# Performance work log

Hardware: AMD Instinct MI355X
Metric: run time of the kernel (lower is better)

## Reference

```python
import jax, jax.numpy as jnp
import numpy as np
import math

D_MODEL = 1024
N_HEADS = 16
D_KV = 64
NUM_BUCKETS = 32
MAX_DISTANCE = 128
BATCH = 4
SEQ = 2048


def _relative_position_bucket(relative_position, num_buckets=NUM_BUCKETS, max_distance=MAX_DISTANCE):
    # bidirectional=True (encoder)
    num_buckets //= 2
    relative_buckets = (relative_position > 0).astype(jnp.int32) * num_buckets
    rp = jnp.abs(relative_position)
    max_exact = num_buckets // 2
    is_small = rp < max_exact
    rp_safe = jnp.maximum(rp, 1)  # avoid log(0); masked by is_small anyway
    rp_if_large = max_exact + (
        jnp.log(rp_safe.astype(jnp.float32) / max_exact)
        / math.log(max_distance / max_exact)
        * (num_buckets - max_exact)
    ).astype(jnp.int32)
    rp_if_large = jnp.minimum(rp_if_large, num_buckets - 1)
    relative_buckets += jnp.where(is_small, rp, rp_if_large)
    return relative_buckets


def compute_bias(rel_bias, q_len, k_len):
    context = jnp.arange(q_len)[:, None]
    memory = jnp.arange(k_len)[None, :]
    buckets = _relative_position_bucket(memory - context)  # [q, k]
    values = rel_bias[buckets]                              # [q, k, h]
    return jnp.transpose(values, (2, 0, 1))[None]           # [1, h, q, k]


def setup_inputs() -> dict:
    key = jax.random.key(0)
    ks = jax.random.split(key, 6)
    s = 1.0 / math.sqrt(D_MODEL)
    return {
        "hidden_states": jax.random.normal(ks[0], (BATCH, SEQ, D_MODEL), jnp.float32),
        "wq": jax.random.normal(ks[1], (D_MODEL, N_HEADS * D_KV), jnp.float32) * s,
        "wk": jax.random.normal(ks[2], (D_MODEL, N_HEADS * D_KV), jnp.float32) * s,
        "wv": jax.random.normal(ks[3], (D_MODEL, N_HEADS * D_KV), jnp.float32) * s,
        "wo": jax.random.normal(ks[4], (N_HEADS * D_KV, D_MODEL), jnp.float32) * s,
        "rel_bias": jax.random.normal(ks[5], (NUM_BUCKETS, N_HEADS), jnp.float32) * 0.5,
    }


def reference(hidden_states, wq, wk, wv, wo, rel_bias):
    B, S, _ = hidden_states.shape

    def shape(x):  # [B,S,H*Dk] -> [B,H,S,Dk]
        return x.reshape(B, S, N_HEADS, D_KV).transpose(0, 2, 1, 3)

    q = shape(hidden_states @ wq)
    k = shape(hidden_states @ wk)
    v = shape(hidden_states @ wv)

    # NOTE: T5 does NOT scale by 1/sqrt(d_kv)
    scores = jnp.einsum("bhqd,bhkd->bhqk", q, k)
    position_bias = compute_bias(rel_bias, S, S)  # [1,H,S,S]
    scores = scores + position_bias
    attn = jax.nn.softmax(scores.astype(jnp.float32), axis=-1).astype(scores.dtype)
    ctx = jnp.einsum("bhqk,bhkd->bhqd", attn, v)
    ctx = ctx.transpose(0, 2, 1, 3).reshape(B, S, N_HEADS * D_KV)
    return ctx @ wo
```

## Files before the change

kernel.cpp:

```cpp
#include <hip/hip_runtime.h>
#include <hip/hip_bf16.h>

typedef unsigned short u16;
typedef unsigned int   u32;
typedef __bf16 bf16x8 __attribute__((ext_vector_type(8)));
typedef float  f32x4  __attribute__((ext_vector_type(4)));
typedef u16    u16x8  __attribute__((ext_vector_type(8)));
typedef u16    u16x4  __attribute__((ext_vector_type(4)));

#define MFMA16(a,b,c) __builtin_amdgcn_mfma_f32_16x16x32_bf16(a,b,c,0,0,0)
#define LOG2E 1.4426950408889634f

__device__ __forceinline__ u16 f2b(float f) {
    u32 u = __builtin_bit_cast(u32, f);
    u32 r = (u + 0x7FFFu + ((u >> 16) & 1u)) >> 16;
    return (u16)r;
}

typedef const __attribute__((address_space(1))) u32* gaddr_t;
typedef __attribute__((address_space(3))) u32*       laddr_t;
__device__ __forceinline__ void gl_lds16(const void* g, void* l) {
    __builtin_amdgcn_global_load_lds((gaddr_t)g, (laddr_t)l, 16, 0, 0);
}

__global__ __launch_bounds__(256) void cast_h_kernel(const float* __restrict__ src,
                                                     u16* __restrict__ dst) {
    int i = (blockIdx.x * 256 + threadIdx.x) * 8;
    float4 a = *(const float4*)(src + i);
    float4 b = *(const float4*)(src + i + 4);
    u16x8 o = { f2b(a.x), f2b(a.y), f2b(a.z), f2b(a.w),
                f2b(b.x), f2b(b.y), f2b(b.z), f2b(b.w) };
    *(u16x8*)(dst + i) = o;
}

__global__ __launch_bounds__(256) void transpose_w_kernel(
        const float* __restrict__ wq, const float* __restrict__ wk,
        const float* __restrict__ wv, const float* __restrict__ wo,
        u16* __restrict__ Wt, u16* __restrict__ Wot) {
    __shared__ u16 tile[64 * 72];
    int g = blockIdx.z;
    const float* src = (g == 0) ? wq : (g == 1) ? wk : (g == 2) ? wv : wo;
    u16* dst = (g < 3) ? (Wt + g * 1048576) : Wot;
    int k0 = blockIdx.x * 64, n0 = blockIdx.y * 64;
    int t = threadIdx.x;
#pragma unroll
    for (int rr = 0; rr < 4; ++rr) {
        int idx = rr * 256 + t;
        int kr = idx >> 4, c = idx & 15;
        float4 v = *(const float4*)(src + (k0 + kr) * 1024 + n0 + c * 4);
        u16x4 o = { f2b(v.x), f2b(v.y), f2b(v.z), f2b(v.w) };
        *(u16x4*)&tile[kr * 72 + c * 4] = o;
    }
    __syncthreads();
#pragma unroll
    for (int rr = 0; rr < 2; ++rr) {
        int idx = rr * 256 + t;
        int n = idx >> 3, c = idx & 7;
        u16x8 o;
#pragma unroll
        for (int j = 0; j < 8; ++j) o[j] = tile[(c * 8 + j) * 72 + n];
        *(u16x8*)(dst + (n0 + n) * 1024 + k0 + c * 8) = o;
    }
}

__global__ __launch_bounds__(256) void bias_kernel(const float* __restrict__ rel_bias,
                                                   float* __restrict__ tab) {
    int i = blockIdx.x * 256 + threadIdx.x;
    int h = i >> 12;
    int idx = i & 4095;
    int delta = idx - 2048;
    int bucket = (delta > 0) ? 16 : 0;
    int rp = delta < 0 ? -delta : delta;
    if (rp < 8) {
        bucket += rp;
    } else {
        double v = log((double)rp / 8.0) / log(16.0) * 8.0;
        int tt = (int)v;
        int b2 = 8 + tt;
        bucket += (b2 < 15) ? b2 : 15;
    }
    tab[h * 4096 + idx] = rel_bias[bucket * 16 + h] * LOG2E;
}

template <int MODE>
__global__ __launch_bounds__(256) void gemm_bt(
        const u16* __restrict__ A, const u16* __restrict__ Bt, int K, int N,
        u16* __restrict__ q_out, u16* __restrict__ k_out, u16* __restrict__ v_out,
        float* __restrict__ f_out) {
    __shared__ u16 As[128 * 32];
    __shared__ u16 Bs[128 * 32];
    int t = threadIdx.x;
    int lane = t & 63, w = t >> 6;
    int wm = w & 1, wn = w >> 1;
    int ln = lane & 15, quad = lane >> 4;
    int m0 = blockIdx.x * 128, n0 = blockIdx.y * 128;
    const u16* Ab = A + m0 * K;
    const u16* Bb = Bt + n0 * K;
    f32x4 acc[4][4] = {};
    int nk = K >> 5;
    for (int kt = 0; kt < nk; ++kt) {
        int k0 = kt * 32;
#pragma unroll
        for (int rr = 0; rr < 2; ++rr) {
            int idx = rr * 256 + t;
            int row = idx >> 2, c = (idx & 3) ^ (row & 3);
            gl_lds16(Ab + row * K + k0 + c * 8, ((char*)As) + idx * 16);
            gl_lds16(Bb + row * K + k0 + c * 8, ((char*)Bs) + idx * 16);
        }
        __syncthreads();
        bf16x8 af[4], bfr[4];
#pragma unroll
        for (int mb = 0; mb < 4; ++mb) {
            int row = wm * 64 + mb * 16 + ln;
            af[mb] = *(const bf16x8*)&As[row * 32 + ((quad ^ (row & 3)) << 3)];
        }
#pragma unroll
        for (int nb = 0; nb < 4; ++nb) {
            int row = wn * 64 + nb * 16 + ln;
            bfr[nb] = *(const bf16x8*)&Bs[row * 32 + ((quad ^ (row & 3)) << 3)];
        }
#pragma unroll
        for (int mb = 0; mb < 4; ++mb)
#pragma unroll
            for (int nb = 0; nb < 4; ++nb)
                acc[mb][nb] = MFMA16(af[mb], bfr[nb], acc[mb][nb]);
        __syncthreads();
    }
#pragma unroll
    for (int mb = 0; mb < 4; ++mb)
#pragma unroll
        for (int nb = 0; nb < 4; ++nb)
#pragma unroll
            for (int r = 0; r < 4; ++r) {
                int m = m0 + wm * 64 + mb * 16 + quad * 4 + r;
                int n = n0 + wn * 64 + nb * 16 + ln;
                float v = acc[mb][nb][r];
                if (MODE == 0) {
                    int which = n >> 10, h = (n >> 6) & 15, d = n & 63;
                    int b = m >> 11, s = m & 2047;
                    u16* dst = (which == 0) ? q_out : (which == 1) ? k_out : v_out;
                    float scale = (which == 0) ? LOG2E : 1.0f;
                    dst[(((b << 4) + h) * 2048 + s) * 64 + d] = f2b(v * scale);
                } else {
                    f_out[m * N + n] = v;
                }
            }
}

__global__ __launch_bounds__(256) void transpose_v_kernel(const u16* __restrict__ Vraw,
                                                          u16* __restrict__ Vt) {
    __shared__ u16 tile[64 * 72];
    int t = threadIdx.x;
    int s0 = blockIdx.x * 64;
    int bh = blockIdx.y;
    const u16* src = Vraw + (bh * 2048 + s0) * 64;
    u16* dst = Vt + bh * 64 * 2048;
#pragma unroll
    for (int rr = 0; rr < 2; ++rr) {
        int idx = rr * 256 + t;
        int s = idx >> 3, c = idx & 7;
        *(u16x8*)&tile[s * 72 + c * 8] = *(const u16x8*)(src + idx * 8);
    }
    __syncthreads();
#pragma unroll
    for (int rr = 0; rr < 2; ++rr) {
        int idx = rr * 256 + t;
        int d = idx >> 3, c = idx & 7;
        u16x8 o;
#pragma unroll
        for (int j = 0; j < 8; ++j) o[j] = tile[(c * 8 + j) * 72 + d];
        *(u16x8*)(dst + d * 2048 + s0 + c * 8) = o;
    }
}

__global__ __launch_bounds__(256, 3) void attn_kernel(
        const u16* __restrict__ Qb, const u16* __restrict__ Kb,
        const u16* __restrict__ Vt, const float* __restrict__ bias_tab,
        u16* __restrict__ ctx) {
    __shared__ u16 Ks[128 * 64];
    __shared__ u16 Vs[64 * 128];
    __shared__ u16 Ps[4][16 * 64];
    __shared__ float sb[2112];
    int t = threadIdx.x;
    int lane = t & 63, w = t >> 6;
    int ln = lane & 15, quad = lane >> 4;
    int bh = blockIdx.x >> 5;
    int qtile = blockIdx.x & 31;
    int h = bh & 15, b = bh >> 4;
    int q0 = qtile * 64;

    float chi = bias_tab[h * 4096 + 2048 + 1500];
    float clo = bias_tab[h * 4096 + 2048 - 1500];

    const float* tb = bias_tab + h * 4096 + (1985 - q0);
    for (int i = t; i < 2111; i += 256) sb[i] = tb[i];

    int qa = q0 + w * 16 + ln;
    const u16* qptr = Qb + (bh * 2048 + qa) * 64 + quad * 8;
    bf16x8 qf0 = *(const bf16x8*)(qptr);
    bf16x8 qf1 = *(const bf16x8*)(qptr + 32);

    const u16* Kbase = Kb + bh * 2048 * 64;
    const u16* Vbase = Vt + bh * 64 * 2048;

    f32x4 oacc[4] = {};
    float l_i = 0.0f;
    int cb_base = 63 - w * 16 + quad * 4 - ln;
    int swl = ln & 7;

    for (int kt = 0; kt < 16; ++kt) {
        int kb0 = kt * 128;
#pragma unroll
        for (int it = 0; it < 4; ++it) {
            int idx = it * 256 + t;
            int row = idx >> 3, c = (idx & 7) ^ (row & 7);
            gl_lds16(Kbase + (kb0 + row) * 64 + c * 8, ((char*)Ks) + idx * 16);
        }
#pragma unroll
        for (int it = 0; it < 4; ++it) {
            int idx = it * 256 + t;
            int row = idx >> 4, c = (idx & 15) ^ (row & 7);
            gl_lds16(Vbase + row * 2048 + kb0 + c * 8, ((char*)Vs) + idx * 16);
        }
        __syncthreads();

        f32x4 sacc[8];
        int diff = kb0 - q0;
        if (diff >= 192 || diff <= -256) {
            float c0 = (diff > 0) ? chi : clo;
            f32x4 ci = {c0, c0, c0, c0};
#pragma unroll
            for (int nb = 0; nb < 8; ++nb) {
                int key = nb * 16 + ln;
                int sw = key & 7;
                bf16x8 kf0 = *(const bf16x8*)&Ks[key * 64 + ((quad ^ sw) << 3)];
                bf16x8 kf1 = *(const bf16x8*)&Ks[key * 64 + (((quad ^ 4) ^ sw) << 3)];
                f32x4 scc = MFMA16(kf0, qf0, ci);
                sacc[nb] = MFMA16(kf1, qf1, scc);
            }
        } else {
            int cb = kb0 + cb_base;
#pragma unroll
            for (int nb = 0; nb < 8; ++nb) {
                int key = nb * 16 + ln;
                int sw = key & 7;
                const float* bp = &sb[cb + nb * 16];
                f32x4 ci = {bp[0], bp[1], bp[2], bp[3]};
                bf16x8 kf0 = *(const bf16x8*)&Ks[key * 64 + ((quad ^ sw) << 3)];
                bf16x8 kf1 = *(const bf16x8*)&Ks[key * 64 + (((quad ^ 4) ^ sw) << 3)];
                f32x4 scc = MFMA16(kf0, qf0, ci);
                sacc[nb] = MFMA16(kf1, qf1, scc);
            }
        }

        float p[8][4];
        float ls0 = 0.f, ls1 = 0.f, ls2 = 0.f, ls3 = 0.f;
#pragma unroll
        for (int nb = 0; nb < 8; ++nb) {
            float e0 = __builtin_amdgcn_exp2f(sacc[nb][0]);
            float e1 = __builtin_amdgcn_exp2f(sacc[nb][1]);
            float e2 = __builtin_amdgcn_exp2f(sacc[nb][2]);
            float e3 = __builtin_amdgcn_exp2f(sacc[nb][3]);
            p[nb][0] = e0; p[nb][1] = e1; p[nb][2] = e2; p[nb][3] = e3;
            ls0 += e0; ls1 += e1; ls2 += e2; ls3 += e3;
        }
        l_i += (ls0 + ls1) + (ls2 + ls3);

        u16* pw = &Ps[w][0];
#pragma unroll
        for (int half = 0; half < 2; ++half) {
#pragma unroll
            for (int nbh = 0; nbh < 4; ++nbh) {
                int nb = half * 4 + nbh;
                u32 a0 = __builtin_bit_cast(u32, p[nb][0]) + 0x8000u;
                u32 a1 = __builtin_bit_cast(u32, p[nb][1]) + 0x8000u;
                u32 a2 = __builtin_bit_cast(u32, p[nb][2]) + 0x8000u;
                u32 a3 = __builtin_bit_cast(u32, p[nb][3]) + 0x8000u;
                u32 lo = __builtin_amdgcn_perm(a1, a0, 0x07060302);
                u32 hi = __builtin_amdgcn_perm(a3, a2, 0x07060302);
                int c = nbh * 2 + (quad >> 1);
                u32* dst = (u32*)&pw[ln * 64 + ((c ^ swl) << 3) + (quad & 1) * 4];
                dst[0] = lo;
                dst[1] = hi;
            }
#pragma unroll
            for (int kc = 0; kc < 2; ++kc) {
                bf16x8 pf = *(const bf16x8*)&pw[ln * 64 + (((kc * 4 + quad) ^ swl) << 3)];
#pragma unroll
                for (int nb = 0; nb < 4; ++nb) {
                    int d = nb * 16 + ln;
                    int vc = (half * 8 + kc * 4 + quad) ^ (d & 7);
                    bf16x8 vf = *(const bf16x8*)&Vs[d * 128 + (vc << 3)];
                    oacc[nb] = MFMA16(pf, vf, oacc[nb]);
                }
            }
        }
        __syncthreads();
    }

    l_i += __shfl_xor(l_i, 16);
    l_i += __shfl_xor(l_i, 32);
    float linv = 1.0f / l_i;
#pragma unroll
    for (int r = 0; r < 4; ++r) {
        float lr = __shfl(linv, quad * 4 + r);
        int q = q0 + w * 16 + quad * 4 + r;
#pragma unroll
        for (int nb = 0; nb < 4; ++nb)
            ctx[(b * 2048 + q) * 1024 + h * 64 + nb * 16 + ln] = f2b(oacc[nb][r] * lr);
    }
}

extern "C" void kernel_launch(void* const* d_in, const int* in_sizes, int n_in,
                              void* d_out, int out_size, void* d_ws, size_t ws_size,
                              hipStream_t stream) {
    const float* H   = (const float*)d_in[0];
    const float* wq  = (const float*)d_in[1];
    const float* wk  = (const float*)d_in[2];
    const float* wv  = (const float*)d_in[3];
    const float* wo  = (const float*)d_in[4];
    const float* rel = (const float*)d_in[5];
    float* out = (float*)d_out;

    char* ws = (char*)d_ws;
    u16* Hb    = (u16*)(ws);
    u16* Wt    = (u16*)(ws + 16777216);
    u16* Wot   = (u16*)(ws + 23068672);
    u16* Qb    = (u16*)(ws + 25165824);
    u16* Kb    = (u16*)(ws + 41943040);
    u16* Vraw  = (u16*)(ws + 58720256);
    float* bias_tab = (float*)(ws + 75497472);
    u16* Vt  = Hb;
    u16* ctx = Vraw;

    cast_h_kernel<<<4096, 256, 0, stream>>>(H, Hb);
    transpose_w_kernel<<<dim3(16, 16, 4), 256, 0, stream>>>(wq, wk, wv, wo, Wt, Wot);
    bias_kernel<<<256, 256, 0, stream>>>(rel, bias_tab);
    gemm_bt<0><<<dim3(64, 24), 256, 0, stream>>>(Hb, Wt, 1024, 3072, Qb, Kb, Vraw, nullptr);
    transpose_v_kernel<<<dim3(32, 64), 256, 0, stream>>>(Vraw, Vt);
    attn_kernel<<<2048, 256, 0, stream>>>(Qb, Kb, Vt, bias_tab, ctx);
    gemm_bt<1><<<dim3(64, 8), 256, 0, stream>>>(ctx, Wot, 1024, 1024, nullptr, nullptr, nullptr, out);
}
```

Baseline: 314.8 us.

## Fuse prep kernels and write V transposed from the QKV GEMM epilogue

Merges the H cast, weight transpose and bias table kernels into one prep kernel launch. The separate V transpose pass goes away: V-column tiles of the QKV GEMM are staged through a new shared-memory tile and written straight out in [d, s] layout with vector stores. This saves two launches and one round trip of V through global memory. The cost is about 34 KB of extra LDS in the MODE 0 GEMM, which may lower occupancy for every QKV block. The attention kernel's bias staging buffer is also made slightly larger.

```diff
diff --git a/kernel.cpp b/kernel.cpp
--- a/kernel.cpp
+++ b/kernel.cpp
@@ -23,63 +23,63 @@
     __builtin_amdgcn_global_load_lds((gaddr_t)g, (laddr_t)l, 16, 0, 0);
 }
 
-__global__ __launch_bounds__(256) void cast_h_kernel(const float* __restrict__ src,
-                                                     u16* __restrict__ dst) {
-    int i = (blockIdx.x * 256 + threadIdx.x) * 8;
-    float4 a = *(const float4*)(src + i);
-    float4 b = *(const float4*)(src + i + 4);
-    u16x8 o = { f2b(a.x), f2b(a.y), f2b(a.z), f2b(a.w),
-                f2b(b.x), f2b(b.y), f2b(b.z), f2b(b.w) };
-    *(u16x8*)(dst + i) = o;
-}
-
-__global__ __launch_bounds__(256) void transpose_w_kernel(
-        const float* __restrict__ wq, const float* __restrict__ wk,
-        const float* __restrict__ wv, const float* __restrict__ wo,
-        u16* __restrict__ Wt, u16* __restrict__ Wot) {
+__global__ __launch_bounds__(256) void prep_kernel(
+        const float* __restrict__ H, const float* __restrict__ wq,
+        const float* __restrict__ wk, const float* __restrict__ wv,
+        const float* __restrict__ wo, const float* __restrict__ rel_bias,
+        u16* __restrict__ Hb, u16* __restrict__ Wt, u16* __restrict__ Wot,
+        float* __restrict__ tab) {
     __shared__ u16 tile[64 * 72];
-    int g = blockIdx.z;
-    const float* src = (g == 0) ? wq : (g == 1) ? wk : (g == 2) ? wv : wo;
-    u16* dst = (g < 3) ? (Wt + g * 1048576) : Wot;
-    int k0 = blockIdx.x * 64, n0 = blockIdx.y * 64;
+    int bi = blockIdx.x;
     int t = threadIdx.x;
-#pragma unroll
-    for (int rr = 0; rr < 4; ++rr) {
-        int idx = rr * 256 + t;
-        int kr = idx >> 4, c = idx & 15;
-        float4 v = *(const float4*)(src + (k0 + kr) * 1024 + n0 + c * 4);
-        u16x4 o = { f2b(v.x), f2b(v.y), f2b(v.z), f2b(v.w) };
-        *(u16x4*)&tile[kr * 72 + c * 4] = o;
-    }
-    __syncthreads();
-#pragma unroll
-    for (int rr = 0; rr < 2; ++rr) {
-        int idx = rr * 256 + t;
-        int n = idx >> 3, c = idx & 7;
-        u16x8 o;
-#pragma unroll
-        for (int j = 0; j < 8; ++j) o[j] = tile[(c * 8 + j) * 72 + n];
-        *(u16x8*)(dst + (n0 + n) * 1024 + k0 + c * 8) = o;
-    }
-}
-
-__global__ __launch_bounds__(256) void bias_kernel(const float* __restrict__ rel_bias,
-                                                   float* __restrict__ tab) {
-    int i = blockIdx.x * 256 + threadIdx.x;
-    int h = i >> 12;
-    int idx = i & 4095;
-    int delta = idx - 2048;
-    int bucket = (delta > 0) ? 16 : 0;
-    int rp = delta < 0 ? -delta : delta;
-    if (rp < 8) {
-        bucket += rp;
+    if (bi < 4096) {
+        int i = (bi * 256 + t) * 8;
+        float4 a = *(const float4*)(H + i);
+        float4 b = *(const float4*)(H + i + 4);
+        u16x8 o = { f2b(a.x), f2b(a.y), f2b(a.z), f2b(a.w),
+                    f2b(b.x), f2b(b.y), f2b(b.z), f2b(b.w) };
+        *(u16x8*)(Hb + i) = o;
+    } else if (bi < 5120) {
+        int g2 = bi - 4096;
+        int g = g2 >> 8, rem = g2 & 255;
+        int n0 = (rem >> 4) * 64, k0 = (rem & 15) * 64;
+        const float* src = (g == 0) ? wq : (g == 1) ? wk : (g == 2) ? wv : wo;
+        u16* dst = (g < 3) ? (Wt + g * 1048576) : Wot;
+#pragma unroll
+        for (int rr = 0; rr < 4; ++rr) {
+            int idx = rr * 256 + t;
+            int kr = idx >> 4, c = idx & 15;
+            float4 v = *(const float4*)(src + (k0 + kr) * 1024 + n0 + c * 4);
+            u16x4 o = { f2b(v.x), f2b(v.y), f2b(v.z), f2b(v.w) };
+            *(u16x4*)&tile[kr * 72 + c * 4] = o;
+        }
+        __syncthreads();
+#pragma unroll
+        for (int rr = 0; rr < 2; ++rr) {
+            int idx = rr * 256 + t;
+            int n = idx >> 3, c = idx & 7;
+            u16x8 o;
+#pragma unroll
+            for (int j = 0; j < 8; ++j) o[j] = tile[(c * 8 + j) * 72 + n];
+            *(u16x8*)(dst + (n0 + n) * 1024 + k0 + c * 8) = o;
+        }
     } else {
-        double v = log((double)rp / 8.0) / log(16.0) * 8.0;
-        int tt = (int)v;
-        int b2 = 8 + tt;
-        bucket += (b2 < 15) ? b2 : 15;
-    }
-    tab[h * 4096 + idx] = rel_bias[bucket * 16 + h] * LOG2E;
+        int i = (bi - 5120) * 256 + t;
+        int h = i >> 12;
+        int idx = i & 4095;
+        int delta = idx - 2048;
+        int bucket = (delta > 0) ? 16 : 0;
+        int rp = delta < 0 ? -delta : delta;
+        if (rp < 8) {
+            bucket += rp;
+        } else {
+            double v = log((double)rp / 8.0) / log(16.0) * 8.0;
+            int tt = (int)v;
+            int b2 = 8 + tt;
+            bucket += (b2 < 15) ? b2 : 15;
+        }
+        tab[h * 4096 + idx] = rel_bias[bucket * 16 + h] * LOG2E;
+    }
 }
 
 template <int MODE>
@@ -89,6 +89,7 @@
         float* __restrict__ f_out) {
     __shared__ u16 As[128 * 32];
     __shared__ u16 Bs[128 * 32];
+    __shared__ u16 vt_tile[MODE == 0 ? 128 * 136 : 1];
     int t = threadIdx.x;
     int lane = t & 63, w = t >> 6;
     int wm = w & 1, wn = w >> 1;
@@ -126,50 +127,51 @@
                 acc[mb][nb] = MFMA16(af[mb], bfr[nb], acc[mb][nb]);
         __syncthreads();
     }
-#pragma unroll
-    for (int mb = 0; mb < 4; ++mb)
-#pragma unroll
-        for (int nb = 0; nb < 4; ++nb)
-#pragma unroll
-            for (int r = 0; r < 4; ++r) {
-                int m = m0 + wm * 64 + mb * 16 + quad * 4 + r;
-                int n = n0 + wn * 64 + nb * 16 + ln;
-                float v = acc[mb][nb][r];
-                if (MODE == 0) {
-                    int which = n >> 10, h = (n >> 6) & 15, d = n & 63;
-                    int b = m >> 11, s = m & 2047;
-                    u16* dst = (which == 0) ? q_out : (which == 1) ? k_out : v_out;
-                    float scale = (which == 0) ? LOG2E : 1.0f;
-                    dst[(((b << 4) + h) * 2048 + s) * 64 + d] = f2b(v * scale);
-                } else {
-                    f_out[m * N + n] = v;
+    if (MODE == 0 && n0 >= 2048) {
+#pragma unroll
+        for (int mb = 0; mb < 4; ++mb)
+#pragma unroll
+            for (int nb = 0; nb < 4; ++nb)
+#pragma unroll
+                for (int r = 0; r < 4; ++r) {
+                    int np = wn * 64 + nb * 16 + ln;
+                    int mp = wm * 64 + mb * 16 + quad * 4 + r;
+                    vt_tile[np * 136 + mp] = f2b(acc[mb][nb][r]);
                 }
-            }
-}
-
-__global__ __launch_bounds__(256) void transpose_v_kernel(const u16* __restrict__ Vraw,
-                                                          u16* __restrict__ Vt) {
-    __shared__ u16 tile[64 * 72];
-    int t = threadIdx.x;
-    int s0 = blockIdx.x * 64;
-    int bh = blockIdx.y;
-    const u16* src = Vraw + (bh * 2048 + s0) * 64;
-    u16* dst = Vt + bh * 64 * 2048;
-#pragma unroll
-    for (int rr = 0; rr < 2; ++rr) {
-        int idx = rr * 256 + t;
-        int s = idx >> 3, c = idx & 7;
-        *(u16x8*)&tile[s * 72 + c * 8] = *(const u16x8*)(src + idx * 8);
-    }
-    __syncthreads();
-#pragma unroll
-    for (int rr = 0; rr < 2; ++rr) {
-        int idx = rr * 256 + t;
-        int d = idx >> 3, c = idx & 7;
-        u16x8 o;
-#pragma unroll
-        for (int j = 0; j < 8; ++j) o[j] = tile[(c * 8 + j) * 72 + d];
-        *(u16x8*)(dst + d * 2048 + s0 + c * 8) = o;
+        __syncthreads();
+        int h0 = (n0 >> 6) & 15;
+        int b = m0 >> 11;
+        int s0 = m0 & 2047;
+#pragma unroll
+        for (int j = 0; j < 8; ++j) {
+            int e = j * 256 + t;
+            int d_all = e >> 4;
+            int sc = e & 15;
+            int hh = h0 + (d_all >> 6);
+            int d = d_all & 63;
+            u16x8 val = *(const u16x8*)&vt_tile[d_all * 136 + sc * 8];
+            *(u16x8*)(v_out + (b * 16 + hh) * 131072 + d * 2048 + s0 + sc * 8) = val;
+        }
+    } else {
+#pragma unroll
+        for (int mb = 0; mb < 4; ++mb)
+#pragma unroll
+            for (int nb = 0; nb < 4; ++nb)
+#pragma unroll
+                for (int r = 0; r < 4; ++r) {
+                    int m = m0 + wm * 64 + mb * 16 + quad * 4 + r;
+                    int n = n0 + wn * 64 + nb * 16 + ln;
+                    float v = acc[mb][nb][r];
+                    if (MODE == 0) {
+                        int which = n >> 10, h = (n >> 6) & 15, d = n & 63;
+                        int b = m >> 11, s = m & 2047;
+                        u16* dst = (which == 0) ? q_out : k_out;
+                        float scale = (which == 0) ? LOG2E : 1.0f;
+                        dst[(((b << 4) + h) * 2048 + s) * 64 + d] = f2b(v * scale);
+                    } else {
+                        f_out[m * N + n] = v;
+                    }
+                }
     }
 }
 
@@ -180,7 +182,7 @@
     __shared__ u16 Ks[128 * 64];
     __shared__ u16 Vs[64 * 128];
     __shared__ u16 Ps[4][16 * 64];
-    __shared__ float sb[2112];
+    __shared__ float sb[2176];
     int t = threadIdx.x;
     int lane = t & 63, w = t >> 6;
     int ln = lane & 15, quad = lane >> 4;
@@ -193,7 +195,7 @@
     float clo = bias_tab[h * 4096 + 2048 - 1500];
 
     const float* tb = bias_tab + h * 4096 + (1985 - q0);
-    for (int i = t; i < 2111; i += 256) sb[i] = tb[i];
+    for (int i = t; i < 2175; i += 256) sb[i] = tb[i];
 
     int qa = q0 + w * 16 + ln;
     const u16* qptr = Qb + (bh * 2048 + qa) * 64 + quad * 8;
@@ -328,16 +330,12 @@
     u16* Wot   = (u16*)(ws + 23068672);
     u16* Qb    = (u16*)(ws + 25165824);
     u16* Kb    = (u16*)(ws + 41943040);
-    u16* Vraw  = (u16*)(ws + 58720256);
+    u16* Vt    = (u16*)(ws + 58720256);
     float* bias_tab = (float*)(ws + 75497472);
-    u16* Vt  = Hb;
-    u16* ctx = Vraw;
-
-    cast_h_kernel<<<4096, 256, 0, stream>>>(H, Hb);
-    transpose_w_kernel<<<dim3(16, 16, 4), 256, 0, stream>>>(wq, wk, wv, wo, Wt, Wot);
-    bias_kernel<<<256, 256, 0, stream>>>(rel, bias_tab);
-    gemm_bt<0><<<dim3(64, 24), 256, 0, stream>>>(Hb, Wt, 1024, 3072, Qb, Kb, Vraw, nullptr);
-    transpose_v_kernel<<<dim3(32, 64), 256, 0, stream>>>(Vraw, Vt);
+    u16* ctx = Hb;
+
+    prep_kernel<<<5376, 256, 0, stream>>>(H, wq, wk, wv, wo, rel, Hb, Wt, Wot, bias_tab);
+    gemm_bt<0><<<dim3(64, 24), 256, 0, stream>>>(Hb, Wt, 1024, 3072, Qb, Kb, Vt, nullptr);
     attn_kernel<<<2048, 256, 0, stream>>>(Qb, Kb, Vt, bias_tab, ctx);
     gemm_bt<1><<<dim3(64, 8), 256, 0, stream>>>(ctx, Wot, 1024, 1024, nullptr, nullptr, nullptr, out);
 }
```

After: 303.2 us. 1.04x faster.
